# Optimization experiments

Measured on AMD Instinct MI355X. Metric: run time of the kernel, lower is better.

## Reference

```python
import jax, jax.numpy as jnp
import numpy as np

MODEL_DIM = 2048
INNER_DIM = 512
NUM_HEADS = 16
FFN_DIM = 8192
MEM_TOKENS = 64
BATCH = 2
SEQ = 2048
EPS = 1e-6


def _rmsnorm(x, w):
    # norm = ||x|| / sqrt(d); out = w * x / (norm + eps)
    norm = jnp.linalg.norm(x, axis=-1, keepdims=True) / np.sqrt(x.shape[-1])
    return w * x / (norm + EPS)


def setup_inputs() -> dict:
    key = jax.random.key(0)
    names_shapes = [
        ("x", (BATCH, SEQ, MODEL_DIM)), ("memory", (BATCH, MEM_TOKENS, MODEL_DIM)),
        ("wq", (MODEL_DIM, MODEL_DIM)), ("wk", (MODEL_DIM, MODEL_DIM)),
        ("wv", (MODEL_DIM, MODEL_DIM)), ("wz", (MODEL_DIM, MODEL_DIM)),
        ("wg", (MODEL_DIM, MODEL_DIM)),
        ("md1", (MODEL_DIM, INNER_DIM)), ("md2", (INNER_DIM, MODEL_DIM)),
        ("mcw", (MODEL_DIM, MODEL_DIM)),
        ("awq", (MODEL_DIM, MODEL_DIM)), ("awk", (MODEL_DIM, MODEL_DIM)),
        ("awv", (MODEL_DIM, MODEL_DIM)), ("awo", (MODEL_DIM, MODEL_DIM)),
        ("f1", (MODEL_DIM, FFN_DIM)), ("f2", (FFN_DIM, MODEL_DIM)),
    ]
    keys = jax.random.split(key, len(names_shapes))
    inp = {}
    for (name, shape), k in zip(names_shapes, keys):
        scale = 1.0 if name in ("x", "memory") else 0.02
        inp[name] = jax.random.normal(k, shape, dtype=jnp.float32) * scale
    for name, dim in [("bq", MODEL_DIM), ("bk", MODEL_DIM), ("bv", MODEL_DIM),
                      ("bz", MODEL_DIM), ("bg", MODEL_DIM), ("mb1", INNER_DIM),
                      ("mb2", MODEL_DIM), ("mcb", MODEL_DIM), ("abq", MODEL_DIM),
                      ("abk", MODEL_DIM), ("abv", MODEL_DIM), ("abo", MODEL_DIM),
                      ("fb1", FFN_DIM), ("fb2", MODEL_DIM)]:
        inp[name] = jnp.zeros((dim,), dtype=jnp.float32)
    inp["n1w"] = jnp.ones((MODEL_DIM,), dtype=jnp.float32)
    inp["n2w"] = jnp.ones((MODEL_DIM,), dtype=jnp.float32)
    return inp


def reference(x, memory, wq, bq, wk, bk, wv, bv, wz, bz, wg, bg, n1w, n2w,
              md1, mb1, md2, mb2, mcw, mcb, awq, abq, awk, abk, awv, abv,
              awo, abo, f1, fb1, f2, fb2):
    B, S, D = x.shape
    H = NUM_HEADS
    dh = D // H

    # 1. projections on RMS-normed input
    xn = _rmsnorm(x, n1w)
    k_ = xn @ wk + bk
    v_ = xn @ wv + bv  # computed as in original (feeds attention path via h_t)
    z = xn @ wz + bz

    # MDI decay gamma: 2-layer decay net + context modulation, sigmoid
    gamma = jax.nn.sigmoid((jax.nn.gelu(z @ md1 + mb1) @ md2 + mb2)
                           + (k_ @ mcw + mcb))

    # 2. associative scan (exponential cumulative product) on contiguous reshape
    g4 = gamma.reshape(B, H, S, dh)  # faithful torch .view semantics
    cumprod = jnp.cumprod(g4, axis=2).reshape(B, S, D)

    # 3-4. core formula: h_t = z_t * sigmoid(W_g h_prev) + gamma * h_prev
    gate = jax.nn.sigmoid(x @ wg + bg)
    h_t = z * gate + gamma * x

    # 5. multi-memory attention: queries from h_t, keys/values from memory bank
    qa = (h_t @ awq + abq).reshape(B, S, H, dh)
    ka = (memory @ awk + abk).reshape(B, -1, H, dh)
    va = (memory @ awv + abv).reshape(B, -1, H, dh)
    scores = jnp.einsum('bshd,bmhd->bhsm', qa, ka) / np.sqrt(dh)
    attn = jax.nn.softmax(scores, axis=-1)
    ctx = jnp.einsum('bhsm,bmhd->bshd', attn, va).reshape(B, S, D)
    mem_context = ctx @ awo + abo

    # 6. residuals (dropout in eval mode = identity)
    x_residual = x + (h_t + mem_context)

    # 7. FFN + residual
    xn2 = _rmsnorm(x_residual, n2w)
    ffn_out = jax.nn.gelu(xn2 @ f1 + fb1) @ f2 + fb2
    output = x_residual + ffn_out
    return output, cumprod
```

## Files before the change

kernel.cpp:

```cpp
#include <hip/hip_runtime.h>
#include <stdint.h>
#include <stddef.h>


#define DEV __device__ __forceinline__

typedef __attribute__((ext_vector_type(8))) short bh8;
typedef __attribute__((ext_vector_type(4))) float f32x4;

typedef __attribute__((address_space(1))) uint32_t gu32;
typedef __attribute__((address_space(3))) uint32_t lu32;

DEV void async16(const void* g, void* l) {
  __builtin_amdgcn_global_load_lds((gu32*)g, (lu32*)l, 16, 0, 0);
}

DEV float b2f(short s) {
  union { float f; uint32_t u; } x;
  x.u = ((uint32_t)(uint16_t)s) << 16;
  return x.f;
}
DEV short f2b(float f) {
  uint32_t u = __float_as_uint(f);
  u += 0x7fffu + ((u >> 16) & 1u);
  return (short)(u >> 16);
}
DEV float sigmoid_f(float x) { return 1.f / (1.f + __expf(-x)); }
DEV float gelu_f(float x) {
  float y = 0.7978845608028654f * (x + 0.044715f * x * x * x);
  float t = 1.f - 2.f / (__expf(2.f * y) + 1.f);
  return 0.5f * x * (1.f + t);
}

template <int EPI>
DEV void epi_store(float v, size_t idx, void* Cv, const void* aux0,
                   const void* aux1, const void* aux2, const void* aux3) {
  if constexpr (EPI == 0) {
    ((short*)Cv)[idx] = f2b(v);
  } else if constexpr (EPI == 1) {
    ((short*)Cv)[idx] = f2b(gelu_f(v));
  } else if constexpr (EPI == 2) {
    ((float*)Cv)[idx] = v;
  } else if constexpr (EPI == 3) {
    ((float*)Cv)[idx] = sigmoid_f(v + ((const float*)aux0)[idx]);
  } else if constexpr (EPI == 4) {
    ((float*)Cv)[idx] = v + ((const float*)aux0)[idx] + b2f(((const short*)aux1)[idx]);
  } else if constexpr (EPI == 5) {
    ((float*)Cv)[idx] = v + ((const float*)aux0)[idx];
  } else {
    const float g = sigmoid_f(v + ((const float*)aux0)[idx]);
    ((float*)Cv)[idx] = g;
    const float xv = ((const float*)aux1)[idx];
    const float zz = b2f(((const short*)aux2)[idx]);
    const float gp = b2f(((const short*)aux3)[idx]);
    short* ht = (short*)((float*)Cv + 8388608);
    ht[idx] = f2b(zz * sigmoid_f(gp) + g * xv);
  }
}

template <int EPI>
__global__ __launch_bounds__(512) void gemm8_k(
    const short* __restrict__ A, const short* __restrict__ Bt,
    const float* __restrict__ bias, void* Cv,
    const void* aux0, const void* aux1, const void* aux2, const void* aux3,
    int M, int N, int K) {
  __shared__ __align__(16) short sL[3 * 24576];
  const int tid  = threadIdx.x;
  const int lane = tid & 63;
  const int wave = tid >> 6;
  const int q = lane >> 4;
  const int r = lane & 15;
  const int wm = wave >> 2;
  const int wn = wave & 3;

  const int nwg = gridDim.x * gridDim.y;
  int flat = blockIdx.y * gridDim.x + blockIdx.x;
  flat = (flat & 7) * (nwg >> 3) + (flat >> 3);
  const int bx = flat % gridDim.x;
  const int by = flat / gridDim.x;
  const int m0 = by * 128;
  const int n0 = bx * 256;

  const int srow = tid >> 3;
  const int sk8  = (tid & 7) ^ (srow & 7);
  const short* pA = A  + (size_t)(m0 + srow) * K + sk8 * 8;
  const short* pB = Bt + (size_t)(n0 + srow) * K + sk8 * 8;
  const size_t K64 = (size_t)64 * K;
  short* dA = &sL[tid * 8];
  short* dB = &sL[8192 + tid * 8];

#define STAGE_B(bi, t) do {                        \
    const short* s_ = pB + (size_t)(t) * 64;       \
    short* d_ = dB + (bi) * 24576;                 \
    async16(s_,           d_);                     \
    async16(s_ + K64,     d_ + 4096);              \
    async16(s_ + 2 * K64, d_ + 8192);              \
    async16(s_ + 3 * K64, d_ + 12288);             \
  } while (0)
#define STAGE_A(bi, t) do {                        \
    const short* s_ = pA + (size_t)(t) * 64;       \
    short* d_ = dA + (bi) * 24576;                 \
    async16(s_,       d_);                         \
    async16(s_ + K64, d_ + 4096);                  \
  } while (0)

  const int swz0 = (q ^ (r & 7)) * 8;
  const int swz1 = ((4 + q) ^ (r & 7)) * 8;
  const int aRow = (wm * 64 + r) * 64;
  const int bRow = 8192 + (wn * 64 + r) * 64;

  f32x4 acc[4][4] = {};
  const int NT = K >> 6;

  STAGE_B(0, 0); STAGE_A(0, 0);
  STAGE_B(1, 1); STAGE_A(1, 1);
  asm volatile("s_waitcnt vmcnt(6)" ::: "memory");
  __builtin_amdgcn_s_barrier();

  int cb = 0;
  for (int t = 0; t < NT; ++t) {
    const short* buf = &sL[cb * 24576];
    const int pb = (cb == 0) ? 2 : cb - 1;
    const bool pf = (t + 2 < NT);

    bh8 af0[4], bf0[4];
#pragma unroll
    for (int i = 0; i < 4; ++i) af0[i] = *(const bh8*)&buf[aRow + i * 1024 + swz0];
#pragma unroll
    for (int j = 0; j < 4; ++j) bf0[j] = *(const bh8*)&buf[bRow + j * 1024 + swz0];
    if (pf) STAGE_B(pb, t + 2);
    __builtin_amdgcn_s_barrier();
    asm volatile("s_waitcnt lgkmcnt(0)" ::: "memory");
    __builtin_amdgcn_sched_barrier(0);
    __builtin_amdgcn_s_setprio(1);
#pragma unroll
    for (int i = 0; i < 4; ++i)
#pragma unroll
      for (int j = 0; j < 4; ++j)
        acc[i][j] = __builtin_amdgcn_mfma_f32_16x16x32_bf16(
            af0[i], bf0[j], acc[i][j], 0, 0, 0);
    __builtin_amdgcn_s_setprio(0);
    __builtin_amdgcn_s_barrier();

    bh8 af1[4], bf1[4];
#pragma unroll
    for (int i = 0; i < 4; ++i) af1[i] = *(const bh8*)&buf[aRow + i * 1024 + swz1];
#pragma unroll
    for (int j = 0; j < 4; ++j) bf1[j] = *(const bh8*)&buf[bRow + j * 1024 + swz1];
    if (pf) STAGE_A(pb, t + 2);
    __builtin_amdgcn_s_barrier();
    asm volatile("s_waitcnt lgkmcnt(0)" ::: "memory");
    __builtin_amdgcn_sched_barrier(0);
    __builtin_amdgcn_s_setprio(1);
#pragma unroll
    for (int i = 0; i < 4; ++i)
#pragma unroll
      for (int j = 0; j < 4; ++j)
        acc[i][j] = __builtin_amdgcn_mfma_f32_16x16x32_bf16(
            af1[i], bf1[j], acc[i][j], 0, 0, 0);
    __builtin_amdgcn_s_setprio(0);

    if (pf) asm volatile("s_waitcnt vmcnt(6)" ::: "memory");
    else    asm volatile("s_waitcnt vmcnt(0)" ::: "memory");
    __builtin_amdgcn_s_barrier();
    cb = (cb == 2) ? 0 : cb + 1;
  }
#undef STAGE_A
#undef STAGE_B

#pragma unroll
  for (int j = 0; j < 4; ++j) {
    const int col = n0 + wn * 64 + j * 16 + r;
    const float bv = bias[col];
#pragma unroll
    for (int i = 0; i < 4; ++i) {
#pragma unroll
      for (int rr = 0; rr < 4; ++rr) {
        const int row = m0 + wm * 64 + i * 16 + q * 4 + rr;
        const size_t idx = (size_t)row * N + col;
        epi_store<EPI>(acc[i][j][rr] + bv, idx, Cv, aux0, aux1, aux2, aux3);
      }
    }
  }
}

__global__ __launch_bounds__(256) void transpose_k(const float* __restrict__ in,
                                                   short* __restrict__ out,
                                                   int R, int C) {
  __shared__ float t[64][68];
  const int tx = threadIdx.x, ty = threadIdx.y;
  const int c0 = blockIdx.x * 64, r0 = blockIdx.y * 64;
#pragma unroll
  for (int yy = 0; yy < 64; yy += 16) {
    const float4 v = *(const float4*)&in[(size_t)(r0 + ty + yy) * C + c0 + tx * 4];
    t[ty + yy][tx * 4 + 0] = v.x;
    t[ty + yy][tx * 4 + 1] = v.y;
    t[ty + yy][tx * 4 + 2] = v.z;
    t[ty + yy][tx * 4 + 3] = v.w;
  }
  __syncthreads();
#pragma unroll
  for (int yy = 0; yy < 64; yy += 16) {
    short4 v;
    v.x = f2b(t[tx * 4 + 0][ty + yy]);
    v.y = f2b(t[tx * 4 + 1][ty + yy]);
    v.z = f2b(t[tx * 4 + 2][ty + yy]);
    v.w = f2b(t[tx * 4 + 3][ty + yy]);
    *(short4*)&out[(size_t)(c0 + ty + yy) * R + r0 + tx * 4] = v;
  }
}

__global__ __launch_bounds__(256) void cvt_k(const float* __restrict__ in,
                                             short* __restrict__ out) {
  const size_t i = ((size_t)blockIdx.x * 256 + threadIdx.x) * 4;
  const float4 v = *(const float4*)(in + i);
  short4 o;
  o.x = f2b(v.x); o.y = f2b(v.y); o.z = f2b(v.z); o.w = f2b(v.w);
  *(short4*)(out + i) = o;
}

__global__ __launch_bounds__(256) void rmsnorm_k(const float* __restrict__ in,
                                                 const float* __restrict__ w,
                                                 short* __restrict__ out,
                                                 short* __restrict__ xbout) {
  const int row = blockIdx.x;
  const int tid = threadIdx.x;
  const size_t base = (size_t)row * 2048;
  float v[8];
  const float* p = in + base + tid * 8;
#pragma unroll
  for (int i = 0; i < 8; ++i) v[i] = p[i];
  if (xbout) {
    short* xo = xbout + base + tid * 8;
#pragma unroll
    for (int i = 0; i < 8; ++i) xo[i] = f2b(v[i]);
  }
  float ss = 0.f;
#pragma unroll
  for (int i = 0; i < 8; ++i) ss += v[i] * v[i];
  for (int off = 32; off; off >>= 1) ss += __shfl_down(ss, off);
  __shared__ float red[4];
  __shared__ float sscale;
  if ((tid & 63) == 0) red[tid >> 6] = ss;
  __syncthreads();
  if (tid == 0) {
    float tot = red[0] + red[1] + red[2] + red[3];
    sscale = 1.f / (sqrtf(tot * (1.f / 2048.f)) + 1e-6f);
  }
  __syncthreads();
  const float scale = sscale;
  short* o = out + base + tid * 8;
#pragma unroll
  for (int i = 0; i < 8; ++i) o[i] = f2b(w[tid * 8 + i] * v[i] * scale);
}

__global__ __launch_bounds__(128) void cumprod1_k(float* __restrict__ gamma,
                                                  float* __restrict__ segprod) {
  const int bx = blockIdx.x;
  const int b = bx >> 7, h = (bx >> 3) & 15, seg = bx & 7;
  size_t base = (size_t)b * 4194304 + (size_t)h * 262144 + (size_t)seg * 256 * 128 + threadIdx.x;
  float acc = 1.f;
  for (int s = 0; s < 256; ++s) {
    acc *= gamma[base + (size_t)s * 128];
    gamma[base + (size_t)s * 128] = acc;
  }
  segprod[(size_t)bx * 128 + threadIdx.x] = acc;
}

__global__ __launch_bounds__(128) void cumprod2_k(const float* __restrict__ gamma,
                                                  const float* __restrict__ segprod,
                                                  float* __restrict__ out) {
  const int bx = blockIdx.x;
  const int b = bx >> 7, h = (bx >> 3) & 15, seg = bx & 7;
  size_t base = (size_t)b * 4194304 + (size_t)h * 262144 + (size_t)seg * 256 * 128 + threadIdx.x;
  float pre = 1.f;
  const size_t sp0 = (size_t)(bx & ~7) * 128 + threadIdx.x;
  for (int t = 0; t < seg; ++t) pre *= segprod[sp0 + (size_t)t * 128];
  for (int s = 0; s < 256; ++s)
    out[base + (size_t)s * 128] = gamma[base + (size_t)s * 128] * pre;
}

__global__ __launch_bounds__(512) void attn_k(const short* __restrict__ qa,
                                              const short* __restrict__ ka,
                                              const short* __restrict__ va,
                                              short* __restrict__ ctx) {
  __shared__ short sk[64][136];
  __shared__ short sv[64][136];
  __shared__ float sq[32][128];
  __shared__ float ss[32][64];
  const int tid = threadIdx.x;
  const int b = blockIdx.z, h = blockIdx.y;
  const int s0 = blockIdx.x * 32;
  const size_t hoff = (size_t)h * 128;
  for (int i = tid; i < 64 * 128; i += 512) {
    int m = i >> 7, d = i & 127;
    sk[m][d] = ka[((size_t)b * 64 + m) * 2048 + hoff + d];
    sv[m][d] = va[((size_t)b * 64 + m) * 2048 + hoff + d];
  }
  for (int i = tid; i < 32 * 128; i += 512) {
    int s = i >> 7, d = i & 127;
    sq[s][d] = b2f(qa[((size_t)b * 2048 + s0 + s) * 2048 + hoff + d]);
  }
  __syncthreads();
  const int g = tid >> 4;
  const int t = tid & 15;
  float sc[4];
#pragma unroll
  for (int mi = 0; mi < 4; ++mi) {
    const int m = mi * 16 + t;
    float a = 0.f;
    for (int d = 0; d < 128; ++d) a += sq[g][d] * b2f(sk[m][d]);
    sc[mi] = a * 0.08838834764831843f;
  }
  float mx = fmaxf(fmaxf(sc[0], sc[1]), fmaxf(sc[2], sc[3]));
#pragma unroll
  for (int off = 8; off; off >>= 1) mx = fmaxf(mx, __shfl_xor(mx, off, 16));
  float sum = 0.f;
#pragma unroll
  for (int mi = 0; mi < 4; ++mi) { sc[mi] = __expf(sc[mi] - mx); sum += sc[mi]; }
#pragma unroll
  for (int off = 8; off; off >>= 1) sum += __shfl_xor(sum, off, 16);
  const float inv = 1.f / sum;
#pragma unroll
  for (int mi = 0; mi < 4; ++mi) ss[g][mi * 16 + t] = sc[mi] * inv;
  __syncthreads();
  const int d0 = t * 8;
  float o[8] = {};
  for (int m = 0; m < 64; ++m) {
    const float wgt = ss[g][m];
#pragma unroll
    for (int i = 0; i < 8; ++i) o[i] += wgt * b2f(sv[m][d0 + i]);
  }
  short* op = ctx + ((size_t)b * 2048 + s0 + g) * 2048 + hoff + d0;
#pragma unroll
  for (int i = 0; i < 8; ++i) op[i] = f2b(o[i]);
}

extern "C" void kernel_launch(void* const* d_in, const int* in_sizes, int n_in,
                              void* d_out, int out_size, void* d_ws, size_t ws_size,
                              hipStream_t stream) {
  (void)in_sizes; (void)n_in; (void)out_size; (void)ws_size;
  const float* x   = (const float*)d_in[0];
  const float* mem = (const float*)d_in[1];
  const float* wk  = (const float*)d_in[3];
  const float* wz  = (const float*)d_in[5];
  const float* wg  = (const float*)d_in[6];
  const float* md1 = (const float*)d_in[7];
  const float* md2 = (const float*)d_in[8];
  const float* mcw = (const float*)d_in[9];
  const float* awq = (const float*)d_in[10];
  const float* awk = (const float*)d_in[11];
  const float* awv = (const float*)d_in[12];
  const float* awo = (const float*)d_in[13];
  const float* f1  = (const float*)d_in[14];
  const float* f2  = (const float*)d_in[15];
  const float* bk  = (const float*)d_in[17];
  const float* bz  = (const float*)d_in[19];
  const float* bg  = (const float*)d_in[20];
  const float* mb1 = (const float*)d_in[21];
  const float* mb2 = (const float*)d_in[22];
  const float* mcb = (const float*)d_in[23];
  const float* abq = (const float*)d_in[24];
  const float* abk = (const float*)d_in[25];
  const float* abv = (const float*)d_in[26];
  const float* abo = (const float*)d_in[27];
  const float* fb1 = (const float*)d_in[28];
  const float* fb2 = (const float*)d_in[29];
  const float* n1w = (const float*)d_in[30];
  const float* n2w = (const float*)d_in[31];

  char* W = (char*)d_ws;
  short* wkT  = (short*)(W + 0);
  short* wzT  = (short*)(W + 8388608);
  short* wgT  = (short*)(W + 16777216);
  short* mcwT = (short*)(W + 25165824);
  short* md1T = (short*)(W + 33554432);
  short* md2T = (short*)(W + 35651584);
  short* awqT = (short*)(W + 37748736);
  short* awkT = (short*)(W + 46137344);
  short* awvT = (short*)(W + 54525952);
  short* awoT = (short*)(W + 62914560);
  short* f1T  = (short*)(W + 71303168);
  short* f2T  = (short*)(W + 104857600);
  char*  big  = W + 138412032;
  short* xn   = (short*)(big + 0);
  short* kk   = (short*)(big + 16777216);
  short* z    = (short*)(big + 33554432);
  short* gpre = (short*)(big + 50331648);
  short* ctx  = kk;
  short* t2   = (short*)big;
  short* t1   = (short*)(W + 205520896);
  float* gamma = (float*)(W + 209715200);
  float* xres  = gamma;
  short* ht   = (short*)(W + 243269632);
  short* qa   = (short*)(W + 260046848);
  short* xn2  = qa;
  short* xb   = (short*)(W + 276824064);
  short* memb = (short*)(W + 293601280);
  short* ka   = (short*)(W + 294125568);
  short* va   = (short*)(W + 294649856);
  float* segprod = (float*)(W + 295174144);

  float* out0 = (float*)d_out;
  float* out1 = out0 + 8388608;

  const dim3 tb16(16, 16);
  transpose_k<<<dim3(32, 32), tb16, 0, stream>>>(wk, wkT, 2048, 2048);
  transpose_k<<<dim3(32, 32), tb16, 0, stream>>>(wz, wzT, 2048, 2048);
  transpose_k<<<dim3(32, 32), tb16, 0, stream>>>(wg, wgT, 2048, 2048);
  transpose_k<<<dim3(32, 32), tb16, 0, stream>>>(mcw, mcwT, 2048, 2048);
  transpose_k<<<dim3(8, 32), tb16, 0, stream>>>(md1, md1T, 2048, 512);
  transpose_k<<<dim3(32, 8), tb16, 0, stream>>>(md2, md2T, 512, 2048);
  transpose_k<<<dim3(32, 32), tb16, 0, stream>>>(awq, awqT, 2048, 2048);
  transpose_k<<<dim3(32, 32), tb16, 0, stream>>>(awk, awkT, 2048, 2048);
  transpose_k<<<dim3(32, 32), tb16, 0, stream>>>(awv, awvT, 2048, 2048);
  transpose_k<<<dim3(32, 32), tb16, 0, stream>>>(awo, awoT, 2048, 2048);
  transpose_k<<<dim3(128, 32), tb16, 0, stream>>>(f1, f1T, 2048, 8192);
  transpose_k<<<dim3(32, 128), tb16, 0, stream>>>(f2, f2T, 8192, 2048);

  cvt_k<<<256, 256, 0, stream>>>(mem, memb);
  rmsnorm_k<<<4096, 256, 0, stream>>>(x, n1w, xn, xb);

  gemm8_k<0><<<dim3(8, 32), 512, 0, stream>>>(xn, wkT, bk, kk, nullptr, nullptr, nullptr, nullptr, 4096, 2048, 2048);
  gemm8_k<0><<<dim3(8, 32), 512, 0, stream>>>(xn, wzT, bz, z, nullptr, nullptr, nullptr, nullptr, 4096, 2048, 2048);
  gemm8_k<0><<<dim3(8, 32), 512, 0, stream>>>(xb, wgT, bg, gpre, nullptr, nullptr, nullptr, nullptr, 4096, 2048, 2048);

  gemm8_k<1><<<dim3(2, 32), 512, 0, stream>>>(z, md1T, mb1, t1, nullptr, nullptr, nullptr, nullptr, 4096, 512, 2048);
  gemm8_k<2><<<dim3(8, 32), 512, 0, stream>>>(t1, md2T, mb2, gamma, nullptr, nullptr, nullptr, nullptr, 4096, 2048, 512);
  gemm8_k<6><<<dim3(8, 32), 512, 0, stream>>>(kk, mcwT, mcb, gamma, gamma, x, z, gpre, 4096, 2048, 2048);

  cumprod1_k<<<256, 128, 0, stream>>>(gamma, segprod);
  cumprod2_k<<<256, 128, 0, stream>>>(gamma, segprod, out1);

  gemm8_k<0><<<dim3(8, 32), 512, 0, stream>>>(ht, awqT, abq, qa, nullptr, nullptr, nullptr, nullptr, 4096, 2048, 2048);
  gemm8_k<0><<<dim3(8, 1), 512, 0, stream>>>(memb, awkT, abk, ka, nullptr, nullptr, nullptr, nullptr, 128, 2048, 2048);
  gemm8_k<0><<<dim3(8, 1), 512, 0, stream>>>(memb, awvT, abv, va, nullptr, nullptr, nullptr, nullptr, 128, 2048, 2048);

  attn_k<<<dim3(64, 16, 2), 512, 0, stream>>>(qa, ka, va, ctx);

  gemm8_k<4><<<dim3(8, 32), 512, 0, stream>>>(ctx, awoT, abo, xres, x, ht, nullptr, nullptr, 4096, 2048, 2048);

  rmsnorm_k<<<4096, 256, 0, stream>>>(xres, n2w, xn2, nullptr);

  gemm8_k<1><<<dim3(32, 32), 512, 0, stream>>>(xn2, f1T, fb1, t2, nullptr, nullptr, nullptr, nullptr, 4096, 8192, 2048);
  gemm8_k<5><<<dim3(8, 32), 512, 0, stream>>>(t2, f2T, fb2, out0, xres, nullptr, nullptr, nullptr, 4096, 2048, 8192);
}
```

Before: 1.257 ms.

## Add 256x256-tile GEMM kernel with split LDS phases for large projections

Adds a new GEMM kernel using 256x256 output tiles (8 waves, each computing 128x64), a triple-buffered LDS pipeline with K-step 32, XCD-aware block remapping, and s_setprio around the MFMA bursts. The large 4096x2048 and FFN GEMMs now use it, which halves the grid along M. The goal is higher arithmetic intensity per block and less global traffic per FLOP. In exchange each block holds a large accumulator register file, fewer blocks are launched (128 for the 2048-wide GEMMs on a chip with many CUs), and occupancy is limited to one block per CU.

Result: slower. 1.721 ms (+36.9%).

```diff
diff --git a/kernel.cpp b/kernel.cpp
--- a/kernel.cpp
+++ b/kernel.cpp
@@ -55,6 +55,128 @@
     const float gp = b2f(((const short*)aux3)[idx]);
     short* ht = (short*)((float*)Cv + 8388608);
     ht[idx] = f2b(zz * sigmoid_f(gp) + g * xv);
+  }
+}
+
+template <int EPI>
+__global__ __launch_bounds__(512, 1) void gemm256_k(
+    const short* __restrict__ A, const short* __restrict__ Bt,
+    const float* __restrict__ bias, void* Cv,
+    const void* aux0, const void* aux1, const void* aux2, const void* aux3,
+    int M, int N, int K) {
+  __shared__ __align__(16) short sL[3 * 16384];
+  const int tid  = threadIdx.x;
+  const int lane = tid & 63;
+  const int wave = tid >> 6;
+  const int q = lane >> 4;
+  const int r = lane & 15;
+  const int wm = wave >> 2;
+  const int wn = wave & 3;
+
+  const int gx = gridDim.x, gy = gridDim.y;
+  const int s = blockIdx.y * gx + blockIdx.x;
+  const int px = (gx > gy) ? 4 : 2;
+  const int qx = gx / px;
+  const int qy = (gy * px) >> 3;
+  const int xcd = s & 7, idx = s >> 3;
+  const int bx = (xcd % px) * qx + idx % qx;
+  const int by = (xcd / px) * qy + idx / qx;
+  const int m0 = by * 256;
+  const int n0 = bx * 256;
+
+  const int srow = tid >> 2;
+  const int sg   = (tid & 3) ^ ((srow >> 1) & 3);
+  const short* pA = A  + (size_t)(m0 + srow) * K + sg * 8;
+  const short* pB = Bt + (size_t)(n0 + srow) * K + sg * 8;
+  const size_t Kr = (size_t)128 * K;
+
+#define STG_A(bi, t) do {                                  \
+    const short* s_ = pA + (size_t)(t) * 32;               \
+    short* d_ = &sL[(bi) * 16384 + tid * 8];               \
+    async16(s_,      d_);                                  \
+    async16(s_ + Kr, d_ + 4096);                           \
+  } while (0)
+#define STG_B(bi, t) do {                                  \
+    const short* s_ = pB + (size_t)(t) * 32;               \
+    short* d_ = &sL[(bi) * 16384 + 8192 + tid * 8];        \
+    async16(s_,      d_);                                  \
+    async16(s_ + Kr, d_ + 4096);                           \
+  } while (0)
+
+  const int swz = (q ^ ((r >> 1) & 3)) * 8;
+  const int aBase = (wm * 128 + r) * 32 + swz;
+  const int bBase = 8192 + (wn * 64 + r) * 32 + swz;
+
+  f32x4 acc[8][4] = {};
+  const int NT = K >> 5;
+
+  STG_A(0, 0); STG_B(0, 0);
+  STG_A(1, 1); STG_B(1, 1);
+  asm volatile("s_waitcnt vmcnt(4)" ::: "memory");
+  __builtin_amdgcn_s_barrier();
+
+  int cb = 0;
+  for (int t = 0; t < NT; ++t) {
+    const short* buf = &sL[cb * 16384];
+    const int pb = (cb == 0) ? 2 : cb - 1;
+    const bool pf = (t + 2 < NT);
+
+    bh8 a0[4], b0[4];
+#pragma unroll
+    for (int i = 0; i < 4; ++i) a0[i] = *(const bh8*)&buf[aBase + i * 512];
+#pragma unroll
+    for (int j = 0; j < 4; ++j) b0[j] = *(const bh8*)&buf[bBase + j * 512];
+    if (pf) STG_A(pb, t + 2);
+    __builtin_amdgcn_s_barrier();
+    asm volatile("s_waitcnt lgkmcnt(0)" ::: "memory");
+    __builtin_amdgcn_sched_barrier(0);
+    __builtin_amdgcn_s_setprio(1);
+#pragma unroll
+    for (int i = 0; i < 4; ++i)
+#pragma unroll
+      for (int j = 0; j < 4; ++j)
+        acc[i][j] = __builtin_amdgcn_mfma_f32_16x16x32_bf16(
+            a0[i], b0[j], acc[i][j], 0, 0, 0);
+    __builtin_amdgcn_s_setprio(0);
+    __builtin_amdgcn_s_barrier();
+
+    bh8 a1[4];
+#pragma unroll
+    for (int i = 0; i < 4; ++i) a1[i] = *(const bh8*)&buf[aBase + (4 + i) * 512];
+    if (pf) STG_B(pb, t + 2);
+    __builtin_amdgcn_s_barrier();
+    asm volatile("s_waitcnt lgkmcnt(0)" ::: "memory");
+    __builtin_amdgcn_sched_barrier(0);
+    __builtin_amdgcn_s_setprio(1);
+#pragma unroll
+    for (int i = 0; i < 4; ++i)
+#pragma unroll
+      for (int j = 0; j < 4; ++j)
+        acc[4 + i][j] = __builtin_amdgcn_mfma_f32_16x16x32_bf16(
+            a1[i], b0[j], acc[4 + i][j], 0, 0, 0);
+    __builtin_amdgcn_s_setprio(0);
+
+    if (pf) asm volatile("s_waitcnt vmcnt(4)" ::: "memory");
+    else    asm volatile("s_waitcnt vmcnt(0)" ::: "memory");
+    __builtin_amdgcn_s_barrier();
+    cb = (cb == 2) ? 0 : cb + 1;
+  }
+#undef STG_A
+#undef STG_B
+
+#pragma unroll
+  for (int j = 0; j < 4; ++j) {
+    const int col = n0 + wn * 64 + j * 16 + r;
+    const float bv = bias[col];
+#pragma unroll
+    for (int i = 0; i < 8; ++i) {
+#pragma unroll
+      for (int rr = 0; rr < 4; ++rr) {
+        const int row = m0 + wm * 128 + i * 16 + q * 4 + rr;
+        const size_t idx = (size_t)row * N + col;
+        epi_store<EPI>(acc[i][j][rr] + bv, idx, Cv, aux0, aux1, aux2, aux3);
+      }
+    }
   }
 }
 
@@ -421,27 +543,27 @@
   cvt_k<<<256, 256, 0, stream>>>(mem, memb);
   rmsnorm_k<<<4096, 256, 0, stream>>>(x, n1w, xn, xb);
 
-  gemm8_k<0><<<dim3(8, 32), 512, 0, stream>>>(xn, wkT, bk, kk, nullptr, nullptr, nullptr, nullptr, 4096, 2048, 2048);
-  gemm8_k<0><<<dim3(8, 32), 512, 0, stream>>>(xn, wzT, bz, z, nullptr, nullptr, nullptr, nullptr, 4096, 2048, 2048);
-  gemm8_k<0><<<dim3(8, 32), 512, 0, stream>>>(xb, wgT, bg, gpre, nullptr, nullptr, nullptr, nullptr, 4096, 2048, 2048);
+  gemm256_k<0><<<dim3(8, 16), 512, 0, stream>>>(xn, wkT, bk, kk, nullptr, nullptr, nullptr, nullptr, 4096, 2048, 2048);
+  gemm256_k<0><<<dim3(8, 16), 512, 0, stream>>>(xn, wzT, bz, z, nullptr, nullptr, nullptr, nullptr, 4096, 2048, 2048);
+  gemm256_k<0><<<dim3(8, 16), 512, 0, stream>>>(xb, wgT, bg, gpre, nullptr, nullptr, nullptr, nullptr, 4096, 2048, 2048);
 
   gemm8_k<1><<<dim3(2, 32), 512, 0, stream>>>(z, md1T, mb1, t1, nullptr, nullptr, nullptr, nullptr, 4096, 512, 2048);
   gemm8_k<2><<<dim3(8, 32), 512, 0, stream>>>(t1, md2T, mb2, gamma, nullptr, nullptr, nullptr, nullptr, 4096, 2048, 512);
-  gemm8_k<6><<<dim3(8, 32), 512, 0, stream>>>(kk, mcwT, mcb, gamma, gamma, x, z, gpre, 4096, 2048, 2048);
+  gemm256_k<6><<<dim3(8, 16), 512, 0, stream>>>(kk, mcwT, mcb, gamma, gamma, x, z, gpre, 4096, 2048, 2048);
 
   cumprod1_k<<<256, 128, 0, stream>>>(gamma, segprod);
   cumprod2_k<<<256, 128, 0, stream>>>(gamma, segprod, out1);
 
-  gemm8_k<0><<<dim3(8, 32), 512, 0, stream>>>(ht, awqT, abq, qa, nullptr, nullptr, nullptr, nullptr, 4096, 2048, 2048);
+  gemm256_k<0><<<dim3(8, 16), 512, 0, stream>>>(ht, awqT, abq, qa, nullptr, nullptr, nullptr, nullptr, 4096, 2048, 2048);
   gemm8_k<0><<<dim3(8, 1), 512, 0, stream>>>(memb, awkT, abk, ka, nullptr, nullptr, nullptr, nullptr, 128, 2048, 2048);
   gemm8_k<0><<<dim3(8, 1), 512, 0, stream>>>(memb, awvT, abv, va, nullptr, nullptr, nullptr, nullptr, 128, 2048, 2048);
 
   attn_k<<<dim3(64, 16, 2), 512, 0, stream>>>(qa, ka, va, ctx);
 
-  gemm8_k<4><<<dim3(8, 32), 512, 0, stream>>>(ctx, awoT, abo, xres, x, ht, nullptr, nullptr, 4096, 2048, 2048);
+  gemm256_k<4><<<dim3(8, 16), 512, 0, stream>>>(ctx, awoT, abo, xres, x, ht, nullptr, nullptr, 4096, 2048, 2048);
 
   rmsnorm_k<<<4096, 256, 0, stream>>>(xres, n2w, xn2, nullptr);
 
-  gemm8_k<1><<<dim3(32, 32), 512, 0, stream>>>(xn2, f1T, fb1, t2, nullptr, nullptr, nullptr, nullptr, 4096, 8192, 2048);
-  gemm8_k<5><<<dim3(8, 32), 512, 0, stream>>>(t2, f2T, fb2, out0, xres, nullptr, nullptr, nullptr, 4096, 2048, 8192);
-}
+  gemm256_k<1><<<dim3(32, 16), 512, 0, stream>>>(xn2, f1T, fb1, t2, nullptr, nullptr, nullptr, nullptr, 4096, 8192, 2048);
+  gemm256_k<5><<<dim3(8, 16), 512, 0, stream>>>(t2, f2T, fb2, out0, xres, nullptr, nullptr, nullptr, 4096, 2048, 8192);
+}
```
